# Optimization experiments

Measured on AMD Instinct MI355X. Metric: run time of the kernel, lower is better.

## Reference

```python
import jax, jax.numpy as jnp
import numpy as np

BN_EPS = 1e-5


def setup_inputs() -> dict:
    key = jax.random.key(0)
    ks = jax.random.split(key, 5)
    B, T, N, C, O, K, E = 2, 4, 50000, 32, 32, 3, 800000
    x = jax.random.normal(ks[0], (B, T, N, C), dtype=jnp.float32)
    edge_index = jax.random.randint(ks[1], (2, E), 0, N, dtype=jnp.int64)
    edge_weight = jax.random.uniform(ks[2], (E,), dtype=jnp.float32)
    W = jax.random.normal(ks[3], (K, C, O), dtype=jnp.float32) * 0.05
    bias = jnp.zeros((O,), dtype=jnp.float32)
    gamma = jnp.ones((O,), dtype=jnp.float32)
    beta = jnp.zeros((O,), dtype=jnp.float32)
    return {"x": x, "edge_index": edge_index, "edge_weight": edge_weight,
            "W": W, "bias": bias, "gamma": gamma, "beta": beta}


def reference(x, edge_index, edge_weight, W, bias, gamma, beta):
    # x: [B, T, N, C]; edge_index: [2, E]; W: [K, C, O]
    B, T, N, C = x.shape
    K = W.shape[0]
    src, dst = edge_index[0], edge_index[1]

    # Scaled Laplacian L_hat = 2L/lambda_max - I with sym norm, lambda_max=2
    # => L_hat = -D^{-1/2} A D^{-1/2} (zero diagonal), PyG ChebConv default.
    deg = jax.ops.segment_sum(edge_weight, src, num_segments=N)
    safe = jnp.where(deg > 0, deg, 1.0)
    dinv = jnp.where(deg > 0, 1.0 / jnp.sqrt(safe), 0.0)
    norm = -dinv[src] * edge_weight * dinv[dst]  # [E]

    # Batch all (b, t) slices together: [N, M, C] with M = B*T
    xn = jnp.transpose(x, (2, 0, 1, 3)).reshape(N, B * T, C)

    def lap(z):  # sparse SpMM applied to every (b,t) slice at once
        return jax.ops.segment_sum(norm[:, None, None] * z[src], dst,
                                   num_segments=N)

    # Chebyshev recursion: T0 = x, T1 = L_hat x, Tk = 2 L_hat T_{k-1} - T_{k-2}
    Tx_prev2 = xn
    out = jnp.einsum('nmc,co->nmo', Tx_prev2, W[0])
    if K > 1:
        Tx_prev = lap(xn)
        out = out + jnp.einsum('nmc,co->nmo', Tx_prev, W[1])
        for k in range(2, K):
            Tx_k = 2.0 * lap(Tx_prev) - Tx_prev2
            out = out + jnp.einsum('nmc,co->nmo', Tx_k, W[k])
            Tx_prev2, Tx_prev = Tx_prev, Tx_k
    out = out + bias  # [N, M, O]

    # BatchNorm1d in training mode, applied per (b,t) slice over nodes,
    # exactly as the original per-slice loop does (biased variance).
    mean = jnp.mean(out, axis=0, keepdims=True)              # [1, M, O]
    var = jnp.mean((out - mean) ** 2, axis=0, keepdims=True)  # [1, M, O]
    y = gamma * (out - mean) * jax.lax.rsqrt(var + BN_EPS) + beta
    y = jax.nn.relu(y)

    return jnp.transpose(y.reshape(N, B, T, -1), (1, 2, 0, 3))  # [B,T,N,O]
```

## Files before the change

### kernel.cpp

```cpp
#include <hip/hip_runtime.h>

#define NNODES 50000
#define NEDGES 800000
#define MB 8
#define CF 32
#define OF 32
#define FPN 256
#define TOTAL_OUT (MB * NNODES * OF)
#define NREP 8
#define CAP 64
#define EB (NEDGES / 256)

typedef unsigned short ushort_t;
typedef unsigned int uint_t;
typedef __attribute__((ext_vector_type(8))) short bf16x8;
typedef __attribute__((ext_vector_type(4))) float f32x4;

__device__ __forceinline__ ushort_t f2bf(float f) {
    uint_t u = __float_as_uint(f);
    u += 0x7FFFu + ((u >> 16) & 1u);
    return (ushort_t)(u >> 16);
}
__device__ __forceinline__ float bflo(uint_t u) { return __uint_as_float(u << 16); }
__device__ __forceinline__ float bfhi(uint_t u) { return __uint_as_float(u & 0xFFFF0000u); }

__device__ __forceinline__ bool detect_is64(const int* ei) {
    int lane = threadIdx.x & 63;
    int v = ei[2 * lane + 1];
    return __ballot(v != 0) == 0ULL;
}

__global__ void __launch_bounds__(256) k_build(const int* __restrict__ ei,
                                               const float* __restrict__ w,
                                               const float* __restrict__ x,
                                               float* __restrict__ deg8,
                                               int* __restrict__ counts,
                                               int2* __restrict__ epack,
                                               ushort_t* __restrict__ xn) {
    int b = blockIdx.x;
    int t = threadIdx.x;
    if (b < EB) {
        bool is64 = detect_is64(ei);
        int e = b * 256 + t;
        int s = is64 ? ei[2 * e] : ei[e];
        int d = is64 ? ei[2 * (NEDGES + e)] : ei[NEDGES + e];
        float wt = w[e];
        int rep = b & (NREP - 1);
        atomicAdd(&deg8[s * NREP + rep], wt);
        int pos = atomicAdd(&counts[d], 1);
        if (pos < CAP) {
            int2 pk;
            pk.x = s;
            pk.y = __float_as_int(wt);
            epack[(size_t)d * CAP + pos] = pk;
        }
    } else {
        int bb = b - EB;
        int lane = t & 63;
        int n = bb * 4 + (t >> 6);
        int m = lane >> 3;
        int c = (4 * lane) & 31;
        const float4 v = *(const float4*)(x + ((size_t)m * NNODES + n) * CF + c);
        uint2 d;
        d.x = (uint_t)f2bf(v.x) | ((uint_t)f2bf(v.y) << 16);
        d.y = (uint_t)f2bf(v.z) | ((uint_t)f2bf(v.w) << 16);
        *(uint2*)(xn + (size_t)n * FPN + 4 * lane) = d;
    }
}

__global__ void k_dinv(const float* __restrict__ deg8, float* __restrict__ dinv) {
    int n = blockIdx.x * blockDim.x + threadIdx.x;
    if (n >= NNODES) return;
    const float4* p = (const float4*)(deg8 + (size_t)n * NREP);
    float4 a = p[0], b = p[1];
    float s = a.x + a.y + a.z + a.w + b.x + b.y + b.z + b.w;
    dinv[n] = (s > 0.0f) ? (1.0f / sqrtf(s)) : 0.0f;
}

template <int PHASE>
__global__ void __launch_bounds__(256) k_spmm(const ushort_t* __restrict__ src,
                                              const ushort_t* __restrict__ xn0,
                                              const int* __restrict__ counts,
                                              const int2* __restrict__ epack,
                                              const float* __restrict__ dinv,
                                              ushort_t* __restrict__ dst) {
    int t = threadIdx.x;
    int lane = t & 63;
    int n = __builtin_amdgcn_readfirstlane(blockIdx.x * 4 + (t >> 6));
    int cnt = min(counts[n], CAP);
    float dn = dinv[n];
    float a0 = 0.0f, a1 = 0.0f, a2 = 0.0f, a3 = 0.0f;
    if (cnt > 0) {
        int j = n * CAP + min(lane, cnt - 1);
        int2 ed = epack[j];
        int cv = ed.x;
        float vw = -dinv[cv] * __int_as_float(ed.y) * dn;
        uint_t vv = __float_as_uint(vw);
        for (int k = 0; k < cnt; k += 16) {
            int sc[16]; float v[16];
            #pragma unroll
            for (int i = 0; i < 16; i++) {
                sc[i] = __builtin_amdgcn_readlane(cv, k + i);
                float vr = __uint_as_float(__builtin_amdgcn_readlane((int)vv, k + i));
                v[i] = (k + i < cnt) ? vr : 0.0f;
            }
            uint2 u[16];
            #pragma unroll
            for (int i = 0; i < 16; i++)
                u[i] = *(const uint2*)(src + (size_t)sc[i] * FPN + 4 * lane);
            #pragma unroll
            for (int i = 0; i < 16; i++) {
                a0 += v[i] * bflo(u[i].x);
                a1 += v[i] * bfhi(u[i].x);
                a2 += v[i] * bflo(u[i].y);
                a3 += v[i] * bfhi(u[i].y);
            }
        }
    }
    if (PHASE == 2) {
        const uint2 xu = *(const uint2*)(xn0 + (size_t)n * FPN + 4 * lane);
        a0 = 2.0f * a0 - bflo(xu.x);
        a1 = 2.0f * a1 - bfhi(xu.x);
        a2 = 2.0f * a2 - bflo(xu.y);
        a3 = 2.0f * a3 - bfhi(xu.y);
    }
    uint2 d;
    d.x = (uint_t)f2bf(a0) | ((uint_t)f2bf(a1) << 16);
    d.y = (uint_t)f2bf(a2) | ((uint_t)f2bf(a3) << 16);
    *(uint2*)(dst + (size_t)n * FPN + 4 * lane) = d;
}

__global__ void k_wprep(const float* __restrict__ W, ushort_t* __restrict__ wbf) {
    int tid = threadIdx.x;
    for (int i = tid; i < 384; i += 256) {
        int k    = i >> 7;
        int rem  = i & 127;
        int oh   = rem >> 6;
        int lane = rem & 63;
        int quad = lane >> 4;
        int colc = lane & 15;
        ushort_t* d = wbf + (size_t)i * 8;
        for (int j = 0; j < 8; j++) {
            int c = quad * 8 + j;
            int o = oh * 16 + colc;
            d[j] = f2bf(W[k * (CF * OF) + c * OF + o]);
        }
    }
}

__global__ void __launch_bounds__(256) k_wfuse(const ushort_t* __restrict__ xn,
                                               const ushort_t* __restrict__ t1,
                                               const ushort_t* __restrict__ t2,
                                               const ushort_t* __restrict__ wbf,
                                               const float* __restrict__ bias,
                                               float* __restrict__ out) {
    int t = threadIdx.x;
    int lane = t & 63;
    int wv = blockIdx.x * 4 + (t >> 6);
    if (wv >= NNODES / 16) return;
    int n0 = wv * 16;
    int quad = lane >> 4, col = lane & 15;

    bf16x8 B[6];
    #pragma unroll
    for (int i = 0; i < 6; i++)
        B[i] = *(const bf16x8*)(wbf + (size_t)(i * 64 + lane) * 8);
    float blo = bias[col], bhi = bias[16 + col];

    size_t aoff = (size_t)(n0 + col) * FPN + quad * 8;
    #pragma unroll
    for (int m = 0; m < 8; m++) {
        bf16x8 A0 = *(const bf16x8*)(xn + aoff + m * 32);
        bf16x8 A1 = *(const bf16x8*)(t1 + aoff + m * 32);
        bf16x8 A2 = *(const bf16x8*)(t2 + aoff + m * 32);
        f32x4 lo = { blo, blo, blo, blo };
        f32x4 hi = { bhi, bhi, bhi, bhi };
        lo = __builtin_amdgcn_mfma_f32_16x16x32_bf16(A0, B[0], lo, 0, 0, 0);
        hi = __builtin_amdgcn_mfma_f32_16x16x32_bf16(A0, B[1], hi, 0, 0, 0);
        lo = __builtin_amdgcn_mfma_f32_16x16x32_bf16(A1, B[2], lo, 0, 0, 0);
        hi = __builtin_amdgcn_mfma_f32_16x16x32_bf16(A1, B[3], hi, 0, 0, 0);
        lo = __builtin_amdgcn_mfma_f32_16x16x32_bf16(A2, B[4], lo, 0, 0, 0);
        hi = __builtin_amdgcn_mfma_f32_16x16x32_bf16(A2, B[5], hi, 0, 0, 0);
        float* ob = out + ((size_t)m * NNODES + n0 + quad * 4) * OF + col;
        #pragma unroll
        for (int r = 0; r < 4; r++) {
            ob[(size_t)r * OF]      = lo[r];
            ob[(size_t)r * OF + 16] = hi[r];
        }
    }
}

__global__ void __launch_bounds__(256) k_stats(const float* __restrict__ out,
                                               float* __restrict__ stats) {
    int m = blockIdx.y;
    int t = threadIdx.x;
    int o4 = t & 7, row = t >> 3;
    int n0 = blockIdx.x * 1024;
    int nend = min(n0 + 1024, NNODES);
    float sx = 0, sy = 0, sz = 0, sw = 0;
    float qx = 0, qy = 0, qz = 0, qw = 0;
    for (int n = n0 + row; n < nend; n += 32) {
        const float4 v = *(const float4*)(out + ((size_t)m * NNODES + n) * OF + o4 * 4);
        sx += v.x; sy += v.y; sz += v.z; sw += v.w;
        qx += v.x * v.x; qy += v.y * v.y; qz += v.z * v.z; qw += v.w * v.w;
    }
    __shared__ float4 sS[256];
    __shared__ float4 sQ[256];
    sS[t] = make_float4(sx, sy, sz, sw);
    sQ[t] = make_float4(qx, qy, qz, qw);
    __syncthreads();
    for (int off = 16; off >= 1; off >>= 1) {
        if (row < off) {
            float4 a = sS[t], b = sS[t + off * 8];
            sS[t] = make_float4(a.x + b.x, a.y + b.y, a.z + b.z, a.w + b.w);
            float4 c = sQ[t], d = sQ[t + off * 8];
            sQ[t] = make_float4(c.x + d.x, c.y + d.y, c.z + d.z, c.w + d.w);
        }
        __syncthreads();
    }
    if (row == 0) {
        float4 s = sS[t], q = sQ[t];
        int base = m * 32 + o4 * 4;
        atomicAdd(&stats[base + 0], s.x);
        atomicAdd(&stats[base + 1], s.y);
        atomicAdd(&stats[base + 2], s.z);
        atomicAdd(&stats[base + 3], s.w);
        atomicAdd(&stats[256 + base + 0], q.x);
        atomicAdd(&stats[256 + base + 1], q.y);
        atomicAdd(&stats[256 + base + 2], q.z);
        atomicAdd(&stats[256 + base + 3], q.w);
    }
}

__global__ void __launch_bounds__(256) k_final(float* __restrict__ out,
                                               const float* __restrict__ stats,
                                               const float* __restrict__ gamma,
                                               const float* __restrict__ beta) {
    int idx4 = blockIdx.x * 256 + threadIdx.x;
    size_t base = (size_t)idx4 * 4;
    int o = (int)(base & 31);
    int m = (int)(base / ((size_t)NNODES * OF));
    int mo = m * 32 + o;
    const float4 sm = *(const float4*)(stats + mo);
    const float4 sq = *(const float4*)(stats + 256 + mo);
    const float4 g  = *(const float4*)(gamma + o);
    const float4 bt = *(const float4*)(beta + o);
    const float inv_n = 1.0f / (float)NNODES;
    float4 v = *(const float4*)(out + base);
    {
        float mean = sm.x * inv_n, var = sq.x * inv_n - mean * mean;
        float sc = g.x * rsqrtf(var + 1e-5f);
        v.x = fmaxf(v.x * sc + (bt.x - sc * mean), 0.0f);
    }
    {
        float mean = sm.y * inv_n, var = sq.y * inv_n - mean * mean;
        float sc = g.y * rsqrtf(var + 1e-5f);
        v.y = fmaxf(v.y * sc + (bt.y - sc * mean), 0.0f);
    }
    {
        float mean = sm.z * inv_n, var = sq.z * inv_n - mean * mean;
        float sc = g.z * rsqrtf(var + 1e-5f);
        v.z = fmaxf(v.z * sc + (bt.z - sc * mean), 0.0f);
    }
    {
        float mean = sm.w * inv_n, var = sq.w * inv_n - mean * mean;
        float sc = g.w * rsqrtf(var + 1e-5f);
        v.w = fmaxf(v.w * sc + (bt.w - sc * mean), 0.0f);
    }
    *(float4*)(out + base) = v;
}

extern "C" void kernel_launch(void* const* d_in, const int* in_sizes, int n_in,
                              void* d_out, int out_size, void* d_ws, size_t ws_size,
                              hipStream_t stream) {
    const float* x     = (const float*)d_in[0];
    const int*   ei    = (const int*)d_in[1];
    const float* w     = (const float*)d_in[2];
    const float* W     = (const float*)d_in[3];
    const float* bias  = (const float*)d_in[4];
    const float* gamma = (const float*)d_in[5];
    const float* beta  = (const float*)d_in[6];
    float* out = (float*)d_out;

    char* p = (char*)d_ws;
    auto alloc = [&](size_t bytes) {
        char* r = p;
        p += (bytes + 511) & ~(size_t)511;
        return r;
    };
    int*      counts = (int*)alloc((size_t)NNODES * 4);
    float*    deg8   = (float*)alloc((size_t)NNODES * NREP * 4);
    float*    stats  = (float*)alloc(512 * 4);
    float*    dinv   = (float*)alloc((size_t)NNODES * 4);
    int2*     epack  = (int2*)alloc((size_t)NNODES * CAP * 8);
    ushort_t* wbf    = (ushort_t*)alloc(384 * 8 * 2);
    ushort_t* xn     = (ushort_t*)alloc((size_t)NNODES * FPN * 2);
    ushort_t* t1     = (ushort_t*)alloc((size_t)NNODES * FPN * 2);
    ushort_t* t2     = (ushort_t*)alloc((size_t)NNODES * FPN * 2);

    size_t zlen = (char*)(stats + 512) - (char*)counts;
    hipMemsetAsync(counts, 0, zlen, stream);

    k_wprep<<<1, 256, 0, stream>>>(W, wbf);
    k_build<<<EB + NNODES / 4, 256, 0, stream>>>(ei, w, x, deg8, counts, epack, xn);
    k_dinv<<<(NNODES + 255) / 256, 256, 0, stream>>>(deg8, dinv);

    k_spmm<1><<<NNODES / 4, 256, 0, stream>>>(xn, xn, counts, epack, dinv, t1);
    k_spmm<2><<<NNODES / 4, 256, 0, stream>>>(t1, xn, counts, epack, dinv, t2);

    int wfblocks = (NNODES / 16 + 3) / 4;
    k_wfuse<<<wfblocks, 256, 0, stream>>>(xn, t1, t2, wbf, bias, out);

    dim3 sgrid((NNODES + 1023) / 1024, MB);
    k_stats<<<sgrid, 256, 0, stream>>>(out, stats);
    k_final<<<TOTAL_OUT / 4 / 256, 256, 0, stream>>>(out, stats, gamma, beta);
}
```

Baseline: 369.8 us.

## Build CSR via two-level binning instead of per-node atomic slot lists

Edge construction now bins edges by destination block: each of 128 workgroups stages entries in shared-memory bins and flushes them in chunks to global bin buffers, and a new kernel turns each bin into a compact CSR with a local prefix scan. SpMM then reads contiguous CSR ranges instead of a padded 64-slot per-node array. The aim is fewer global atomics on per-node counters, less memory for edge storage, and better locality in the build. The cost is an extra kernel launch, serialized flushes by a single thread per bin, only 128 edge workgroups, and a hard cap of 9216 entries per bin.

Result: slower. 392.1 us (+6.0%).

```diff
diff --git a/kernel.cpp b/kernel.cpp
--- a/kernel.cpp
+++ b/kernel.cpp
@@ -8,8 +8,15 @@
 #define FPN 256
 #define TOTAL_OUT (MB * NNODES * OF)
 #define NREP 8
-#define CAP 64
-#define EB (NEDGES / 256)
+
+#define BSH 9
+#define BINW 512
+#define NB ((NNODES + BINW - 1) / BINW)
+#define BINCAP 9216
+#define NBB 128
+#define EPB (NEDGES / NBB)
+#define CAPL 32
+#define CH 16
 
 typedef unsigned short ushort_t;
 typedef unsigned int uint_t;
@@ -34,28 +41,59 @@
                                                const float* __restrict__ w,
                                                const float* __restrict__ x,
                                                float* __restrict__ deg8,
-                                               int* __restrict__ counts,
-                                               int2* __restrict__ epack,
+                                               int* __restrict__ g_bin_cnt,
+                                               int2* __restrict__ binbuf,
                                                ushort_t* __restrict__ xn) {
-    int b = blockIdx.x;
+    int blk = blockIdx.x;
     int t = threadIdx.x;
-    if (b < EB) {
+    __shared__ int l_cnt[NB];
+    __shared__ int2 l_buf[NB][CAPL];
+    if (blk < NBB) {
         bool is64 = detect_is64(ei);
-        int e = b * 256 + t;
-        int s = is64 ? ei[2 * e] : ei[e];
-        int d = is64 ? ei[2 * (NEDGES + e)] : ei[NEDGES + e];
-        float wt = w[e];
-        int rep = b & (NREP - 1);
-        atomicAdd(&deg8[s * NREP + rep], wt);
-        int pos = atomicAdd(&counts[d], 1);
-        if (pos < CAP) {
-            int2 pk;
-            pk.x = s;
-            pk.y = __float_as_int(wt);
-            epack[(size_t)d * CAP + pos] = pk;
+        for (int i = t; i < NB; i += 256) l_cnt[i] = 0;
+        __syncthreads();
+        int e0 = blk * EPB;
+        int eend = e0 + EPB;
+        for (int base = e0; base < eend; base += 256) {
+            int e = base + t;
+            if (e < eend) {
+                int s = is64 ? ei[2 * e] : ei[e];
+                int d = is64 ? ei[2 * (NEDGES + e)] : ei[NEDGES + e];
+                float wt = w[e];
+                atomicAdd(&deg8[s * NREP + ((e >> 8) & 7)], wt);
+                int bin = d >> BSH;
+                int2 entry;
+                entry.x = s | ((d & (BINW - 1)) << 16);
+                entry.y = __float_as_int(wt);
+                int pos = atomicAdd(&l_cnt[bin], 1);
+                if (pos < CAPL) {
+                    l_buf[bin][pos] = entry;
+                } else {
+                    int gp = atomicAdd(&g_bin_cnt[bin], 1);
+                    if (gp < BINCAP) binbuf[(size_t)bin * BINCAP + gp] = entry;
+                }
+            }
+            __syncthreads();
+            bool last = (base + 256 >= eend);
+            if (t < NB) {
+                int c = min(l_cnt[t], CAPL);
+                int nflush = last ? c : (c & ~(CH - 1));
+                if (nflush > 0) {
+                    int gp = atomicAdd(&g_bin_cnt[t], nflush);
+                    int2* dst = binbuf + (size_t)t * BINCAP;
+                    for (int i = 0; i < nflush; i++) {
+                        int p = gp + i;
+                        if (p < BINCAP) dst[p] = l_buf[t][i];
+                    }
+                }
+                int r = c - nflush;
+                for (int i = 0; i < r; i++) l_buf[t][i] = l_buf[t][nflush + i];
+                l_cnt[t] = r;
+            }
+            __syncthreads();
         }
     } else {
-        int bb = b - EB;
+        int bb = blk - NBB;
         int lane = t & 63;
         int n = bb * 4 + (t >> 6);
         int m = lane >> 3;
@@ -68,6 +106,71 @@
     }
 }
 
+__global__ void __launch_bounds__(256) k_csr(const int* __restrict__ g_bin_cnt,
+                                             const int2* __restrict__ binbuf,
+                                             int2* __restrict__ csr,
+                                             int* __restrict__ csr_off) {
+    __shared__ int l_ncnt[BINW];
+    __shared__ int l_off[BINW];
+    __shared__ int l_ws[4];
+    __shared__ int l_red[4];
+    int b = blockIdx.x;
+    int t = threadIdx.x;
+    int lane = t & 63, wv = t >> 6;
+
+    int vb = (t < b) ? min(g_bin_cnt[t], BINCAP) : 0;
+    #pragma unroll
+    for (int off = 32; off >= 1; off >>= 1) vb += __shfl_down(vb, off);
+    if (lane == 0) l_red[wv] = vb;
+    l_ncnt[t] = 0;
+    l_ncnt[t + 256] = 0;
+    __syncthreads();
+    int base = l_red[0] + l_red[1] + l_red[2] + l_red[3];
+
+    int cnt = min(g_bin_cnt[b], BINCAP);
+    const int2* bp = binbuf + (size_t)b * BINCAP;
+    for (int i = t; i < cnt; i += 256) {
+        int dl = bp[i].x >> 16;
+        atomicAdd(&l_ncnt[dl], 1);
+    }
+    __syncthreads();
+
+    int a0 = l_ncnt[2 * t], a1 = l_ncnt[2 * t + 1];
+    int psum = a0 + a1;
+    int v = psum;
+    #pragma unroll
+    for (int off = 1; off < 64; off <<= 1) {
+        int u = __shfl_up(v, off);
+        if (lane >= off) v += u;
+    }
+    if (lane == 63) l_ws[wv] = v;
+    __syncthreads();
+    int wpre = 0;
+    for (int i = 0; i < wv; i++) wpre += l_ws[i];
+    int excl = wpre + v - psum;
+    l_off[2 * t] = excl;
+    l_off[2 * t + 1] = excl + a0;
+    __syncthreads();
+
+    int n0 = b * BINW;
+    for (int i = t; i < BINW; i += 256) {
+        int n = n0 + i;
+        if (n < NNODES) csr_off[n] = base + l_off[i];
+    }
+    if (b == NB - 1 && t == 0) csr_off[NNODES] = base + cnt;
+    __syncthreads();
+
+    for (int i = t; i < cnt; i += 256) {
+        int2 e = bp[i];
+        int dl = e.x >> 16;
+        int slot = atomicAdd(&l_off[dl], 1);
+        int2 o;
+        o.x = e.x & 0xFFFF;
+        o.y = e.y;
+        csr[(size_t)base + slot] = o;
+    }
+}
+
 __global__ void k_dinv(const float* __restrict__ deg8, float* __restrict__ dinv) {
     int n = blockIdx.x * blockDim.x + threadIdx.x;
     if (n >= NNODES) return;
@@ -80,19 +183,20 @@
 template <int PHASE>
 __global__ void __launch_bounds__(256) k_spmm(const ushort_t* __restrict__ src,
                                               const ushort_t* __restrict__ xn0,
-                                              const int* __restrict__ counts,
-                                              const int2* __restrict__ epack,
+                                              const int* __restrict__ csr_off,
+                                              const int2* __restrict__ csr,
                                               const float* __restrict__ dinv,
                                               ushort_t* __restrict__ dst) {
     int t = threadIdx.x;
     int lane = t & 63;
     int n = __builtin_amdgcn_readfirstlane(blockIdx.x * 4 + (t >> 6));
-    int cnt = min(counts[n], CAP);
+    int off = csr_off[n];
+    int cnt = min(csr_off[n + 1] - off, 64);
     float dn = dinv[n];
     float a0 = 0.0f, a1 = 0.0f, a2 = 0.0f, a3 = 0.0f;
     if (cnt > 0) {
-        int j = n * CAP + min(lane, cnt - 1);
-        int2 ed = epack[j];
+        int j = off + min(lane, cnt - 1);
+        int2 ed = csr[j];
         int cv = ed.x;
         float vw = -dinv[cv] * __int_as_float(ed.y) * dn;
         uint_t vv = __float_as_uint(vw);
@@ -288,25 +392,28 @@
         p += (bytes + 511) & ~(size_t)511;
         return r;
     };
-    int*      counts = (int*)alloc((size_t)NNODES * 4);
+    int*      g_bin_cnt = (int*)alloc((size_t)NB * 4);
     float*    deg8   = (float*)alloc((size_t)NNODES * NREP * 4);
     float*    stats  = (float*)alloc(512 * 4);
     float*    dinv   = (float*)alloc((size_t)NNODES * 4);
-    int2*     epack  = (int2*)alloc((size_t)NNODES * CAP * 8);
+    int2*     binbuf = (int2*)alloc((size_t)NB * BINCAP * 8);
+    int2*     csr    = (int2*)alloc((size_t)NEDGES * 8);
+    int*      csr_off= (int*)alloc((size_t)(NNODES + 1) * 4);
     ushort_t* wbf    = (ushort_t*)alloc(384 * 8 * 2);
     ushort_t* xn     = (ushort_t*)alloc((size_t)NNODES * FPN * 2);
     ushort_t* t1     = (ushort_t*)alloc((size_t)NNODES * FPN * 2);
     ushort_t* t2     = (ushort_t*)alloc((size_t)NNODES * FPN * 2);
 
-    size_t zlen = (char*)(stats + 512) - (char*)counts;
-    hipMemsetAsync(counts, 0, zlen, stream);
+    size_t zlen = (char*)(stats + 512) - (char*)g_bin_cnt;
+    hipMemsetAsync(g_bin_cnt, 0, zlen, stream);
 
     k_wprep<<<1, 256, 0, stream>>>(W, wbf);
-    k_build<<<EB + NNODES / 4, 256, 0, stream>>>(ei, w, x, deg8, counts, epack, xn);
+    k_build<<<NBB + NNODES / 4, 256, 0, stream>>>(ei, w, x, deg8, g_bin_cnt, binbuf, xn);
     k_dinv<<<(NNODES + 255) / 256, 256, 0, stream>>>(deg8, dinv);
-
-    k_spmm<1><<<NNODES / 4, 256, 0, stream>>>(xn, xn, counts, epack, dinv, t1);
-    k_spmm<2><<<NNODES / 4, 256, 0, stream>>>(t1, xn, counts, epack, dinv, t2);
+    k_csr<<<NB, 256, 0, stream>>>(g_bin_cnt, binbuf, csr, csr_off);
+
+    k_spmm<1><<<NNODES / 4, 256, 0, stream>>>(xn, xn, csr_off, csr, dinv, t1);
+    k_spmm<2><<<NNODES / 4, 256, 0, stream>>>(t1, xn, csr_off, csr, dinv, t2);
 
     int wfblocks = (NNODES / 16 + 3) / 4;
     k_wfuse<<<wfblocks, 256, 0, stream>>>(xn, t1, t2, wbf, bias, out);
```
